# Kernel optimization log

Hardware: AMD Instinct MI355X
Metric: run time of the kernel (lower is better)

The kernel has to match this reference:

```python
import jax, jax.numpy as jnp
import numpy as np

DIM = 128
CODEBOOK_SIZE = 1024
DECAY = 0.99
EPSILON = 1e-06


def setup_inputs() -> dict:
    key = jax.random.key(0)
    k1, k2, k3, k4 = jax.random.split(key, 4)
    x = jax.random.normal(k1, (64, 1024, DIM), dtype=jnp.float32)
    embed = jax.random.normal(k2, (CODEBOOK_SIZE, DIM), dtype=jnp.float32)
    # keep all codes above the dead-code threshold (2) so expire_codes_ is a no-op
    cluster_size = jax.random.uniform(k3, (CODEBOOK_SIZE,), dtype=jnp.float32) * 10.0 + 2.0
    embed_avg = jax.random.normal(k4, (CODEBOOK_SIZE, DIM), dtype=jnp.float32)
    return {"x": x, "embed": embed, "cluster_size": cluster_size, "embed_avg": embed_avg}


def reference(x, embed, cluster_size, embed_avg):
    shape = x.shape
    xf = x.reshape(-1, shape[-1])  # [N, D]

    # quantize: squared euclidean distances [N, K] then argmin
    dist = (
        jnp.sum(xf * xf, axis=1, keepdims=True)
        - 2.0 * (xf @ embed.T)
        + jnp.sum(embed * embed, axis=1)[None, :]
    )
    embed_ind_flat = jnp.argmin(dist, axis=-1)  # [N]
    embed_ind = embed_ind_flat.reshape(shape[:-1])

    # dequantize
    quantize = embed[embed_ind]  # [..., D]

    # training EMA updates (one-hot scatter accumulation)
    one_hot_sum = jax.ops.segment_sum(
        jnp.ones_like(embed_ind_flat, dtype=x.dtype), embed_ind_flat,
        num_segments=CODEBOOK_SIZE)
    embed_sum = jax.ops.segment_sum(xf, embed_ind_flat, num_segments=CODEBOOK_SIZE)  # [K, D]

    cluster_size_new = cluster_size * DECAY + one_hot_sum * (1.0 - DECAY)
    embed_avg_new = embed_avg * DECAY + embed_sum * (1.0 - DECAY)

    total = jnp.sum(cluster_size_new)
    smoothed = (cluster_size_new + EPSILON) / (total + EPSILON * CODEBOOK_SIZE) * total
    embed_new = embed_avg_new / smoothed[:, None]

    return quantize, embed_ind, cluster_size_new, embed_avg_new, embed_new
```

## Files before the change

kernel.cpp:

```cpp
#include <hip/hip_runtime.h>
#include <hip/hip_fp16.h>
#include <float.h>

#define DIMD   128
#define KCODES 1024
#define NROWS  65536
#define TAU    0.032f
#define SEG_R  16

typedef __attribute__((ext_vector_type(8)))  _Float16 half8;
typedef __attribute__((ext_vector_type(16))) float f32x16;

union U8 { uint4 u; half8 h; };

__device__ __forceinline__ unsigned packh2(float a, float b) {
    __half2 t = __floats2half2_rn(a, b);
    return *(unsigned*)&t;
}

__device__ __forceinline__ void stage16(const uint4* g, uint4* l) {
    auto* gp = (const __attribute__((address_space(1))) uint4*)g;
    auto* lp = (__attribute__((address_space(3))) uint4*)l;
    __builtin_amdgcn_global_load_lds(gp, lp, 16, 0, 0);
}

__global__ __launch_bounds__(256) void pre_kernel(
    const float* __restrict__ embed, uint4* __restrict__ ehg,
    float* __restrict__ enorm, uint4* __restrict__ zero_region)
{
    if (blockIdx.x < 64) {
        int t = blockIdx.x * 256 + threadIdx.x;
        int chunk = t >> 9;
        int s = (t >> 6) & 7;
        int L = t & 63;
        const float* src = embed + ((size_t)(chunk * 32 + (L & 31)) * DIMD) + s * 16 + (L >> 5) * 8;
        float4 a = *(const float4*)src;
        float4 b = *(const float4*)(src + 4);
        float f[8] = {a.x, a.y, a.z, a.w, b.x, b.y, b.z, b.w};
        uint4 H;
        unsigned* hw = (unsigned*)&H;
#pragma unroll
        for (int j = 0; j < 4; ++j) hw[j] = packh2(f[2 * j], f[2 * j + 1]);
        ehg[t] = H;
    } else if (blockIdx.x < 68) {
        int k = (blockIdx.x - 64) * 256 + threadIdx.x;
        const float4* e = (const float4*)(embed + (size_t)k * DIMD);
        float s = 0.f;
#pragma unroll
        for (int c = 0; c < DIMD / 4; ++c) {
            float4 v = e[c];
            s += v.x * v.x + v.y * v.y + v.z * v.z + v.w * v.w;
        }
        enorm[k] = s;
    } else {
        uint4 z = {0, 0, 0, 0};
        zero_region[threadIdx.x] = z;
        zero_region[threadIdx.x + 256] = z;
    }
}

__global__ __launch_bounds__(256, 2) void argmin_mfma(
    const float* __restrict__ x, const uint4* __restrict__ ehg,
    const float* __restrict__ enorm,
    int* __restrict__ ind_i, float* __restrict__ ind_f,
    int* __restrict__ wl, int* __restrict__ wl_cnt)
{
    __shared__ uint4 Bs[2][512];
    __shared__ float Es[KCODES];

    const int tid  = threadIdx.x;
    const int wave = tid >> 6;
    const int lane = tid & 63;
    const int n    = lane & 31;
    const int h    = lane >> 5;
    const int row0 = blockIdx.x * 128;
    const int rowA = row0 + wave * 32 + n;

    stage16(ehg + tid,       &Bs[0][tid]);
    stage16(ehg + tid + 256, &Bs[0][tid + 256]);
    ((float4*)Es)[tid] = ((const float4*)enorm)[tid];

    half8 xh[8], xl[8];
    const float* xrow = x + (size_t)rowA * DIMD + h * 8;
#pragma unroll
    for (int s = 0; s < 8; ++s) {
        float4 a = *(const float4*)(xrow + s * 16);
        float4 b = *(const float4*)(xrow + s * 16 + 4);
        float f[8] = {a.x, a.y, a.z, a.w, b.x, b.y, b.z, b.w};
        U8 th, tl;
        unsigned* ph = (unsigned*)&th.u;
        unsigned* pl = (unsigned*)&tl.u;
#pragma unroll
        for (int j = 0; j < 4; ++j) {
            float u0 = f[2 * j], u1 = f[2 * j + 1];
            __half2 hh = __floats2half2_rn(u0, u1);
            ph[j] = *(unsigned*)&hh;
            float2 back = __half22float2(hh);
            __half2 ll = __floats2half2_rn(u0 - back.x, u1 - back.y);
            pl[j] = *(unsigned*)&ll;
        }
        xh[s] = th.h; xl[s] = tl.h;
    }

    int bestv[16], best2[16];
#pragma unroll
    for (int r = 0; r < 16; ++r) { bestv[r] = 0x7FFFFFFF; best2[r] = 0x7FFFFFFF; }

    for (int chunk = 0; chunk < KCODES / 32; ++chunk) {
        const int cur = chunk & 1;
        __syncthreads();
        if (chunk < KCODES / 32 - 1) {
            const uint4* gN = ehg + (chunk + 1) * 512;
            stage16(gN + tid,       &Bs[cur ^ 1][tid]);
            stage16(gN + tid + 256, &Bs[cur ^ 1][tid + 256]);
        }

        float ee_val = Es[(chunk << 5) + n];

        const half8* Bh = (const half8*)Bs[cur];
        half8 bh[8];
#pragma unroll
        for (int s = 0; s < 8; ++s) bh[s] = Bh[s * 64 + lane];

        f32x16 acc;
#pragma unroll
        for (int r = 0; r < 16; ++r) acc[r] = 0.f;
#pragma unroll
        for (int s = 0; s < 8; ++s) {
            acc = __builtin_amdgcn_mfma_f32_32x32x16_f16(xh[s], bh[s], acc, 0, 0, 0);
            acc = __builtin_amdgcn_mfma_f32_32x32x16_f16(xl[s], bh[s], acc, 0, 0, 0);
        }

#pragma unroll
        for (int r = 0; r < 16; ++r) {
            float d = fmaf(-2.f, acc[r], ee_val);
            int p = (int)((__float_as_int(d) & 0xFFFFFFE0u) | (unsigned)chunk);
            int old = bestv[r];
            bestv[r] = min(old, p);
            best2[r] = min(best2[r], max(old, p));
        }
    }

    float fv[16], f2[16];
    int   bi[16];
#pragma unroll
    for (int r = 0; r < 16; ++r) {
        fv[r] = __int_as_float((int)(bestv[r] & 0xFFFFFFE0u));
        f2[r] = __int_as_float((int)(best2[r] & 0xFFFFFFE0u));
        bi[r] = ((bestv[r] & 31) << 5) | n;
    }

#pragma unroll
    for (int m = 1; m <= 16; m <<= 1) {
#pragma unroll
        for (int r = 0; r < 16; ++r) {
            float ov = __shfl_xor(fv[r], m, 64);
            float o2 = __shfl_xor(f2[r], m, 64);
            int   oi = __shfl_xor(bi[r], m, 64);
            float hi = fmaxf(fv[r], ov);
            f2[r] = fminf(fminf(f2[r], o2), hi);
            bool take = (ov < fv[r]) || (ov == fv[r] && oi < bi[r]);
            fv[r] = take ? ov : fv[r];
            bi[r] = take ? oi : bi[r];
        }
    }

    if (n == 0) {
#pragma unroll
        for (int r = 0; r < 16; ++r) {
            int row = row0 + wave * 32 + (r & 3) + 8 * (r >> 2) + 4 * h;
            ind_i[row] = bi[r];
            ind_f[row] = (float)bi[r];
            if (f2[r] - fv[r] < TAU) {
                int p = atomicAdd(wl_cnt, 1);
                if (p < NROWS) wl[p] = row;
            }
        }
    }
}

__global__ __launch_bounds__(256) void recheck_kernel(
    const float* __restrict__ x, const float* __restrict__ embed,
    const float* __restrict__ enorm, const int* __restrict__ wl,
    const int* __restrict__ wl_cnt, int* __restrict__ ind_i, float* __restrict__ ind_f)
{
    __shared__ float xs[DIMD];
    __shared__ float rv[256];
    __shared__ int   ri[256];
    const int tid = threadIdx.x;
    int count = *wl_cnt;
    if (count > NROWS) count = NROWS;

    for (int i = blockIdx.x; i < count; i += gridDim.x) {
        const int row = wl[i];
        __syncthreads();
        if (tid < DIMD) xs[tid] = x[(size_t)row * DIMD + tid];
        __syncthreads();

        const float4* xs4 = (const float4*)xs;
        float xn = 0.f;
#pragma unroll 8
        for (int c = 0; c < 32; ++c) {
            float4 v = xs4[c];
            xn += v.x * v.x + v.y * v.y + v.z * v.z + v.w * v.w;
        }

        float bv = FLT_MAX; int bi = 0;
#pragma unroll
        for (int c = 0; c < 4; ++c) {
            int code = tid * 4 + c;
            const float4* er = (const float4*)(embed + (size_t)code * DIMD);
            float acc = 0.f;
#pragma unroll 8
            for (int kk = 0; kk < 32; ++kk) {
                float4 a = xs4[kk];
                float4 b = er[kk];
                acc += a.x * b.x + a.y * b.y + a.z * b.z + a.w * b.w;
            }
            float d = (xn - 2.0f * acc) + enorm[code];
            if (d < bv) { bv = d; bi = code; }
        }
        rv[tid] = bv; ri[tid] = bi;
        __syncthreads();
        for (int s = 128; s > 0; s >>= 1) {
            if (tid < s) {
                if (rv[tid + s] < rv[tid] || (rv[tid + s] == rv[tid] && ri[tid + s] < ri[tid])) {
                    rv[tid] = rv[tid + s]; ri[tid] = ri[tid + s];
                }
            }
            __syncthreads();
        }
        if (tid == 0) {
            int s_new = ri[0];
            if (s_new != ind_i[row]) {
                ind_i[row] = s_new;
                ind_f[row] = (float)s_new;
            }
        }
        __syncthreads();
    }
}

__global__ __launch_bounds__(256) void hist_kernel(
    const int* __restrict__ ind, int* __restrict__ counts)
{
    __shared__ int hcnt[KCODES];
    for (int i = threadIdx.x; i < KCODES; i += 256) hcnt[i] = 0;
    __syncthreads();
    const int base = blockIdx.x * 2048;
    for (int i = threadIdx.x; i < 2048; i += 256) atomicAdd(&hcnt[ind[base + i]], 1);
    __syncthreads();
    for (int i = threadIdx.x; i < KCODES; i += 256) {
        int v = hcnt[i];
        if (v) atomicAdd(&counts[i], v);
    }
}

__global__ __launch_bounds__(1024) void scan_cluster_kernel(
    const int* __restrict__ counts, const float* __restrict__ cluster_size,
    int* __restrict__ cursor, float* __restrict__ out_cs, float* __restrict__ smoothed)
{
    __shared__ int   s[KCODES];
    __shared__ float rf[KCODES];
    const int t = threadIdx.x;
    int my = counts[t];
    s[t] = my;
    float cs = cluster_size[t] * 0.99f + (float)my * 0.01f;
    out_cs[t] = cs;
    rf[t] = cs;
    __syncthreads();
    for (int d = 1; d < KCODES; d <<= 1) {
        int v = (t >= d) ? s[t - d] : 0;
        __syncthreads();
        s[t] += v;
        __syncthreads();
    }
    cursor[t] = s[t] - my;
    for (int st = 512; st > 0; st >>= 1) {
        if (t < st) rf[t] += rf[t + st];
        __syncthreads();
    }
    float total = rf[0];
    smoothed[t] = (cs + 1e-6f) / (total + 1e-6f * (float)KCODES) * total;
}

__global__ __launch_bounds__(256) void permbuild_kernel(
    const int* __restrict__ ind, int* __restrict__ cursor,
    int* __restrict__ perm, int* __restrict__ codes, uint4* __restrict__ embed_sum4)
{
    const int tid = threadIdx.x;
    if (tid < 128) {
        uint4 z = {0, 0, 0, 0};
        embed_sum4[blockIdx.x * 128 + tid] = z;
    }
    const int row = blockIdx.x * 256 + tid;
    const int k = ind[row];
    int pos = atomicAdd(&cursor[k], 1);
    perm[pos] = row;
    codes[pos] = k;
}

__global__ __launch_bounds__(256) void segsum_kernel(
    const float* __restrict__ x, const float* __restrict__ embed,
    const int* __restrict__ perm, const int* __restrict__ codes,
    float* __restrict__ embed_sum, float* __restrict__ out_q)
{
    const int g = (blockIdx.x * 256 + threadIdx.x) >> 5;
    const int c = threadIdx.x & 31;
    const int base = g * SEG_R;

    float4 acc = {0.f, 0.f, 0.f, 0.f};
    int curk = codes[base];
#pragma unroll
    for (int j = 0; j < SEG_R; ++j) {
        int r = perm[base + j];
        int k = codes[base + j];
        float4 v = *(const float4*)(x + (size_t)r * DIMD + c * 4);
        float4 e = *(const float4*)(embed + (size_t)k * DIMD + c * 4);
        *(float4*)(out_q + (size_t)r * DIMD + c * 4) = e;
        if (k != curk) {
            float* dst = embed_sum + (size_t)curk * DIMD + c * 4;
            atomicAdd(dst + 0, acc.x);
            atomicAdd(dst + 1, acc.y);
            atomicAdd(dst + 2, acc.z);
            atomicAdd(dst + 3, acc.w);
            acc = v;
            curk = k;
        } else {
            acc.x += v.x; acc.y += v.y; acc.z += v.z; acc.w += v.w;
        }
    }
    float* dst = embed_sum + (size_t)curk * DIMD + c * 4;
    atomicAdd(dst + 0, acc.x);
    atomicAdd(dst + 1, acc.y);
    atomicAdd(dst + 2, acc.z);
    atomicAdd(dst + 3, acc.w);
}

__global__ void embed_kernel(
    const float* __restrict__ embed_avg, const float* __restrict__ embed_sum,
    const float* __restrict__ smoothed, float* __restrict__ out_ea,
    float* __restrict__ out_en)
{
    int i = blockIdx.x * blockDim.x + threadIdx.x;
    if (i < KCODES * DIMD) {
        float ea = embed_avg[i] * 0.99f + embed_sum[i] * 0.01f;
        out_ea[i] = ea;
        out_en[i] = ea / smoothed[i >> 7];
    }
}

extern "C" void kernel_launch(void* const* d_in, const int* in_sizes, int n_in,
                              void* d_out, int out_size, void* d_ws, size_t ws_size,
                              hipStream_t stream) {
    const float* x            = (const float*)d_in[0];
    const float* embed        = (const float*)d_in[1];
    const float* cluster_size = (const float*)d_in[2];
    const float* embed_avg    = (const float*)d_in[3];

    float* out     = (float*)d_out;
    float* out_q   = out;
    float* out_ind = out + 8388608;
    float* out_cs  = out + 8454144;
    float* out_ea  = out + 8455168;
    float* out_en  = out + 8586240;

    char* ws = (char*)d_ws;
    int*   ind_i     = (int*)(ws + 0);
    float* enorm     = (float*)(ws + 262144);
    int*   countsI   = (int*)(ws + 266240);
    int*   wl_cnt    = (int*)(ws + 270336);
    int*   cursor    = (int*)(ws + 274432);
    float* smoothed  = (float*)(ws + 278528);
    int*   perm      = (int*)(ws + 286720);
    int*   wl        = (int*)(ws + 548864);
    int*   codes     = (int*)(ws + 548864);
    uint4* ehg       = (uint4*)(ws + 811008);
    float* embed_sum = (float*)(ws + 811008);

    pre_kernel<<<69, 256, 0, stream>>>(embed, ehg, enorm, (uint4*)countsI);
    argmin_mfma<<<NROWS / 128, 256, 0, stream>>>(
        x, ehg, enorm, ind_i, out_ind, wl, wl_cnt);
    recheck_kernel<<<512, 256, 0, stream>>>(
        x, embed, enorm, wl, wl_cnt, ind_i, out_ind);
    hist_kernel<<<32, 256, 0, stream>>>(ind_i, countsI);
    scan_cluster_kernel<<<1, 1024, 0, stream>>>(countsI, cluster_size, cursor, out_cs, smoothed);
    permbuild_kernel<<<NROWS / 256, 256, 0, stream>>>(
        ind_i, cursor, perm, codes, (uint4*)embed_sum);
    segsum_kernel<<<(NROWS / SEG_R) * 32 / 256, 256, 0, stream>>>(
        x, embed, perm, codes, embed_sum, out_q);
    embed_kernel<<<(KCODES * DIMD + 255) / 256, 256, 0, stream>>>(
        embed_avg, embed_sum, smoothed, out_ea, out_en);
}
```

Before: 261.0 us.

## Split codebook across wave pairs and fold distance offset into MFMA accumulator

Each block now handles 64 rows, and each row group's two waves scan different halves of the codebook. Their per-row best and second-best results are merged through shared memory. The -2 scale is folded into the half-precision codebook and the accumulator is seeded with the code norm, which removes the per-element FMA. Launch bounds are raised to 4 waves/SIMD to get more occupancy. The double-buffered prefetch is replaced by a single staged load with two barriers per iteration, so load latency is no longer overlapped with compute. Scaling the codes by -2 before the fp16 conversion changes rounding slightly.

Result: slower. 733.2 us (+181.0%).

```diff
diff --git a/kernel.cpp b/kernel.cpp
--- a/kernel.cpp
+++ b/kernel.cpp
@@ -40,7 +40,7 @@
         uint4 H;
         unsigned* hw = (unsigned*)&H;
 #pragma unroll
-        for (int j = 0; j < 4; ++j) hw[j] = packh2(f[2 * j], f[2 * j + 1]);
+        for (int j = 0; j < 4; ++j) hw[j] = packh2(-2.f * f[2 * j], -2.f * f[2 * j + 1]);
         ehg[t] = H;
     } else if (blockIdx.x < 68) {
         int k = (blockIdx.x - 64) * 256 + threadIdx.x;
@@ -59,25 +59,28 @@
     }
 }
 
-__global__ __launch_bounds__(256, 2) void argmin_mfma(
+__global__ __launch_bounds__(256, 4) void argmin_mfma(
     const float* __restrict__ x, const uint4* __restrict__ ehg,
     const float* __restrict__ enorm,
     int* __restrict__ ind_i, float* __restrict__ ind_f,
     int* __restrict__ wl, int* __restrict__ wl_cnt)
 {
-    __shared__ uint4 Bs[2][512];
+    __shared__ uint4 Bs[1024];
     __shared__ float Es[KCODES];
+    __shared__ float smv[4][32];
+    __shared__ float sm2[4][32];
+    __shared__ int   smi[4][32];
 
     const int tid  = threadIdx.x;
-    const int wave = tid >> 6;
+    const int w    = tid >> 6;
     const int lane = tid & 63;
     const int n    = lane & 31;
     const int h    = lane >> 5;
-    const int row0 = blockIdx.x * 128;
-    const int rowA = row0 + wave * 32 + n;
-
-    stage16(ehg + tid,       &Bs[0][tid]);
-    stage16(ehg + tid + 256, &Bs[0][tid + 256]);
+    const int rg   = w >> 1;
+    const int kh   = w & 1;
+    const int row0 = blockIdx.x * 64;
+    const int rowA = row0 + rg * 32 + n;
+
     ((float4*)Es)[tid] = ((const float4*)enorm)[tid];
 
     half8 xh[8], xl[8];
@@ -106,25 +109,29 @@
 #pragma unroll
     for (int r = 0; r < 16; ++r) { bestv[r] = 0x7FFFFFFF; best2[r] = 0x7FFFFFFF; }
 
-    for (int chunk = 0; chunk < KCODES / 32; ++chunk) {
-        const int cur = chunk & 1;
-        __syncthreads();
-        if (chunk < KCODES / 32 - 1) {
-            const uint4* gN = ehg + (chunk + 1) * 512;
-            stage16(gN + tid,       &Bs[cur ^ 1][tid]);
-            stage16(gN + tid + 256, &Bs[cur ^ 1][tid + 256]);
-        }
-
-        float ee_val = Es[(chunk << 5) + n];
-
-        const half8* Bh = (const half8*)Bs[cur];
+    for (int t = 0; t < 16; ++t) {
+        __syncthreads();
+        {
+            const uint4* g0 = ehg + (size_t)t * 512;
+            const uint4* g1 = ehg + (size_t)(t + 16) * 512;
+            stage16(g0 + tid,        &Bs[tid]);
+            stage16(g0 + tid + 256,  &Bs[tid + 256]);
+            stage16(g1 + tid,        &Bs[512 + tid]);
+            stage16(g1 + tid + 256,  &Bs[512 + tid + 256]);
+        }
+        __syncthreads();
+
+        const int ch = t + kh * 16;
+        float ee_val = Es[(ch << 5) + n];
+
+        const half8* Bh = (const half8*)(Bs + kh * 512);
         half8 bh[8];
 #pragma unroll
         for (int s = 0; s < 8; ++s) bh[s] = Bh[s * 64 + lane];
 
         f32x16 acc;
 #pragma unroll
-        for (int r = 0; r < 16; ++r) acc[r] = 0.f;
+        for (int r = 0; r < 16; ++r) acc[r] = ee_val;
 #pragma unroll
         for (int s = 0; s < 8; ++s) {
             acc = __builtin_amdgcn_mfma_f32_32x32x16_f16(xh[s], bh[s], acc, 0, 0, 0);
@@ -133,8 +140,7 @@
 
 #pragma unroll
         for (int r = 0; r < 16; ++r) {
-            float d = fmaf(-2.f, acc[r], ee_val);
-            int p = (int)((__float_as_int(d) & 0xFFFFFFE0u) | (unsigned)chunk);
+            int p = (int)((__float_as_int(acc[r]) & 0xFFFFFFE0u) | (unsigned)ch);
             int old = bestv[r];
             bestv[r] = min(old, p);
             best2[r] = min(best2[r], max(old, p));
@@ -168,13 +174,29 @@
     if (n == 0) {
 #pragma unroll
         for (int r = 0; r < 16; ++r) {
-            int row = row0 + wave * 32 + (r & 3) + 8 * (r >> 2) + 4 * h;
-            ind_i[row] = bi[r];
-            ind_f[row] = (float)bi[r];
-            if (f2[r] - fv[r] < TAU) {
-                int p = atomicAdd(wl_cnt, 1);
-                if (p < NROWS) wl[p] = row;
-            }
+            int rl = (r & 3) + 8 * (r >> 2) + 4 * h;
+            smv[w][rl] = fv[r];
+            sm2[w][rl] = f2[r];
+            smi[w][rl] = bi[r];
+        }
+    }
+    __syncthreads();
+
+    if (kh == 0 && lane < 32) {
+        const int rl = lane;
+        float va = smv[w][rl],     vb = smv[w ^ 1][rl];
+        float sa = sm2[w][rl],     sb = sm2[w ^ 1][rl];
+        int   ia = smi[w][rl],     ib = smi[w ^ 1][rl];
+        bool tb = (vb < va) || (vb == va && ib < ia);
+        float bv = tb ? vb : va;
+        int   bx = tb ? ib : ia;
+        float second = fminf(fmaxf(va, vb), fminf(sa, sb));
+        int row = row0 + rg * 32 + rl;
+        ind_i[row] = bx;
+        ind_f[row] = (float)bx;
+        if (second - bv < TAU) {
+            int p = atomicAdd(wl_cnt, 1);
+            if (p < NROWS) wl[p] = row;
         }
     }
 }
@@ -379,7 +401,7 @@
     float* embed_sum = (float*)(ws + 811008);
 
     pre_kernel<<<69, 256, 0, stream>>>(embed, ehg, enorm, (uint4*)countsI);
-    argmin_mfma<<<NROWS / 128, 256, 0, stream>>>(
+    argmin_mfma<<<NROWS / 64, 256, 0, stream>>>(
         x, ehg, enorm, ind_i, out_ind, wl, wl_cnt);
     recheck_kernel<<<512, 256, 0, stream>>>(
         x, embed, enorm, wl, wl_cnt, ind_i, out_ind);
```
